# Optimization experiments

Measured on AMD Instinct MI355X. Metric: run time of the kernel, lower is better.

The kernel has to match this reference:

```python
import jax, jax.numpy as jnp
import numpy as np

GROUPS = 8
EPS = 1e-5


def setup_inputs() -> dict:
    key = jax.random.key(0)
    ks = jax.random.split(key, 5)
    b, c, h, w = 16, 512, 64, 64
    x = jax.random.normal(ks[0], (b, c, h, w), dtype=jnp.float32)
    norm_w = jnp.ones((c,), dtype=jnp.float32)
    norm_b = jnp.zeros((c,), dtype=jnp.float32)
    # 1x1 conv weights stored as [out, in] (kernel spatial dims are 1)
    qkv_w = jax.random.normal(ks[1], (3 * c, c), dtype=jnp.float32) * (c ** -0.5)
    qkv_b = jax.random.normal(ks[2], (3 * c,), dtype=jnp.float32) * 0.02
    proj_w = jax.random.normal(ks[3], (c, c), dtype=jnp.float32) * (c ** -0.5)
    proj_b = jax.random.normal(ks[4], (c,), dtype=jnp.float32) * 0.02
    return {"x": x, "norm_w": norm_w, "norm_b": norm_b,
            "qkv_w": qkv_w, "qkv_b": qkv_b, "proj_w": proj_w, "proj_b": proj_b}


def reference(x, norm_w, norm_b, qkv_w, qkv_b, proj_w, proj_b):
    b, c, h, w = x.shape
    n = h * w
    # GroupNorm over (c/groups, h, w) per group, affine per channel
    xg = x.reshape(b, GROUPS, -1)
    mean = xg.mean(axis=-1, keepdims=True)
    var = xg.var(axis=-1, keepdims=True)
    xn = ((xg - mean) * jax.lax.rsqrt(var + EPS)).reshape(b, c, n)
    xn = xn * norm_w[None, :, None] + norm_b[None, :, None]
    # 1x1 conv qkv: [b, 3c, n]
    qkv = jnp.einsum('oc,bcn->bon', qkv_w, xn) + qkv_b[None, :, None]
    qkv = qkv.reshape(b, 3, c, n)
    q, k, v = qkv[:, 0], qkv[:, 1], qkv[:, 2]  # each [b, c, n]
    scale = jnp.asarray(c, x.dtype) ** -0.5
    # NOTE: as in the source, attention is over channels: attn is [b, c, c]
    attn = jnp.einsum('bcn,bdn->bcd', q, k) * scale
    attn = jax.nn.softmax(attn, axis=-1)
    out = jnp.einsum('bcd,bdn->bcn', attn, v)  # [b, c, n]
    out = jnp.einsum('oc,bcn->bon', proj_w, out) + proj_b[None, :, None]
    return x + out.reshape(b, c, h, w)
```

## Files before the change

kernel.cpp:

```cpp
#include <hip/hip_runtime.h>
#include <hip/hip_bf16.h>

using bf16 = __hip_bfloat16;
typedef __attribute__((ext_vector_type(8))) short short8;
typedef __attribute__((ext_vector_type(4))) float f32x4;
typedef __attribute__((ext_vector_type(4))) short short4v;

#define B_   16
#define C_   512
#define N_   4096
#define NG   8
#define GRP_ELEMS (64 * 4096)
static constexpr float kScale = 0.04419417382415922f;
#define SPART_STRIDE 4194304ULL

#define OFF_WQ    0ULL
#define OFF_WP    0x180000ULL
#define OFF_PART  0x204000ULL
#define OFF_SUM   0x210000ULL
#define OFF_CHS   0x218000ULL
#define OFF_U     0x220000ULL
#define OFF_W     0x230000ULL
#define OFF_WVT   0x240000ULL
#define OFF_BV2   0x2C0000ULL
#define OFF_Q     0x400000ULL
#define OFF_K     (OFF_Q  + 0x4000000ULL)
#define OFF_VT    (OFF_K  + 0x4000000ULL)
#define OFF_XNC   OFF_Q
#define OFF_G2    OFF_Q
#define OFF_P     (OFF_Q + 0x1000000ULL)
#define OFF_ATT   (OFF_Q + 0x2000000ULL)
#define OFF_GP    OFF_K
#define OFF_W2    OFF_K
#define OFF_W3    (OFF_K + 0x800000ULL)

typedef __attribute__((address_space(1))) const void* as1cvp;
typedef __attribute__((address_space(3))) void* as3vp;

__device__ inline void gload_lds16(const void* g, void* l) {
  __builtin_amdgcn_global_load_lds((as1cvp)g, (as3vp)l, 16, 0, 0);
}

__device__ inline short bf16bits(float v) {
  bf16 h = __float2bfloat16(v);
  return *reinterpret_cast<short*>(&h);
}

#define BARX() __builtin_amdgcn_s_barrier()
#define SFEN() __builtin_amdgcn_sched_barrier(0)
#define LG0()  asm volatile("s_waitcnt lgkmcnt(0)" ::: "memory")
#define VM4()  asm volatile("s_waitcnt vmcnt(4)" ::: "memory")
#define VM0()  asm volatile("s_waitcnt vmcnt(0)" ::: "memory")

__global__ __launch_bounds__(256) void prep(const float* __restrict__ wq,
                                            const float* __restrict__ wp,
                                            const float* __restrict__ x,
                                            bf16* __restrict__ oq,
                                            bf16* __restrict__ op,
                                            bf16* __restrict__ wvt,
                                            float* __restrict__ part,
                                            float* __restrict__ chansum) {
  if (blockIdx.x < 3072) {
    int i = blockIdx.x * 256 + threadIdx.x;
    oq[i] = __float2bfloat16(wq[i]);
    if (i < 512 * 512) {
      op[i] = __float2bfloat16(wp[i]);
      const int d = i >> 9, c = i & 511;
      wvt[c * 512 + d] = __float2bfloat16(wq[(1024 + d) * 512 + c]);
    }
    return;
  }
  const int bid = blockIdx.x - 3072;
  const int bg  = bid >> 4;
  const int seg = bid & 15;
  const float4* p = (const float4*)(x + (size_t)bg * GRP_ELEMS + seg * 16384);
  float a[4] = {0.f, 0.f, 0.f, 0.f};
  float q = 0.f;
#pragma unroll
  for (int i = 0; i < 16; ++i) {
    float4 v = p[threadIdx.x + i * 256];
    a[i >> 2] += v.x + v.y + v.z + v.w;
    q += v.x * v.x + v.y * v.y + v.z * v.z + v.w * v.w;
  }
  for (int off = 32; off; off >>= 1) {
#pragma unroll
    for (int j = 0; j < 4; ++j) a[j] += __shfl_xor(a[j], off);
    q += __shfl_xor(q, off);
  }
  __shared__ float red[4][5];
  int w = threadIdx.x >> 6;
  if ((threadIdx.x & 63) == 0) {
#pragma unroll
    for (int j = 0; j < 4; ++j) red[w][j] = a[j];
    red[w][4] = q;
  }
  __syncthreads();
  if (threadIdx.x == 0) {
    float c0 = red[0][0] + red[1][0] + red[2][0] + red[3][0];
    float c1 = red[0][1] + red[1][1] + red[2][1] + red[3][1];
    float c2 = red[0][2] + red[1][2] + red[2][2] + red[3][2];
    float c3 = red[0][3] + red[1][3] + red[2][3] + red[3][3];
    float Q  = red[0][4] + red[1][4] + red[2][4] + red[3][4];
    part[bid * 2]     = c0 + c1 + c2 + c3;
    part[bid * 2 + 1] = Q;
    const int b = bg >> 3, c = (bg & 7) * 64 + seg * 4;
    float* cs = chansum + b * 512 + c;
    cs[0] = c0; cs[1] = c1; cs[2] = c2; cs[3] = c3;
  }
}

__global__ __launch_bounds__(256) void gn_apply_t(const float* __restrict__ x,
                                                  const float* __restrict__ part,
                                                  const float* __restrict__ nw,
                                                  const float* __restrict__ nb,
                                                  bf16* __restrict__ xnt,
                                                  bf16* __restrict__ xncn) {
  const int nt = blockIdx.x;
  const int ct = blockIdx.y;
  const int b  = blockIdx.z;
  __shared__ float tile[64][65];
  const int bg = b * NG + ct;
  float Sm = 0.f, Qm = 0.f;
#pragma unroll
  for (int i = 0; i < 16; ++i) {
    Sm += part[(bg * 16 + i) * 2];
    Qm += part[(bg * 16 + i) * 2 + 1];
  }
  const float mean = Sm * (1.f / GRP_ELEMS);
  const float var  = Qm * (1.f / GRP_ELEMS) - mean * mean;
  const float rstd = rsqrtf(var + 1e-5f);

  const int r16 = threadIdx.x >> 4;
  const int q4  = (threadIdx.x & 15) * 4;
#pragma unroll
  for (int p = 0; p < 4; ++p) {
    const int cl = p * 16 + r16;
    const int c  = ct * 64 + cl;
    const float g  = nw[c] * rstd;
    const float sh = nb[c] - mean * g;
    float4 v = *(const float4*)(x + ((size_t)b * C_ + c) * N_ + nt * 64 + q4);
    const float x0 = v.x * g + sh, x1 = v.y * g + sh;
    const float x2 = v.z * g + sh, x3 = v.w * g + sh;
    tile[cl][q4] = x0; tile[cl][q4 + 1] = x1;
    tile[cl][q4 + 2] = x2; tile[cl][q4 + 3] = x3;
    short4v s4 = {bf16bits(x0), bf16bits(x1), bf16bits(x2), bf16bits(x3)};
    *(short4v*)(xncn + ((size_t)b * C_ + c) * N_ + nt * 64 + q4) = s4;
  }
  __syncthreads();
#pragma unroll
  for (int p = 0; p < 4; ++p) {
    const int nl = p * 16 + r16;
    short4v s4 = {bf16bits(tile[q4][nl]), bf16bits(tile[q4 + 1][nl]),
                  bf16bits(tile[q4 + 2][nl]), bf16bits(tile[q4 + 3][nl])};
    *(short4v*)(xnt + ((size_t)b * N_ + nt * 64 + nl) * C_ + ct * 64 + q4) = s4;
  }
}

__global__ __launch_bounds__(512) void mk_ssum(const float* __restrict__ chansum,
                                               const float* __restrict__ part,
                                               const float* __restrict__ nw,
                                               const float* __restrict__ nb,
                                               float* __restrict__ ssum) {
  const int b = blockIdx.x, c = threadIdx.x;
  const int bg = b * NG + (c >> 6);
  float Sm = 0.f, Qm = 0.f;
#pragma unroll
  for (int i = 0; i < 16; ++i) {
    Sm += part[(bg * 16 + i) * 2];
    Qm += part[(bg * 16 + i) * 2 + 1];
  }
  const float mean = Sm * (1.f / GRP_ELEMS);
  const float var  = Qm * (1.f / GRP_ELEMS) - mean * mean;
  const float rstd = rsqrtf(var + 1e-5f);
  const float g  = nw[c] * rstd;
  const float sh = nb[c] - mean * g;
  ssum[b * 512 + c] = g * chansum[b * 512 + c] + 4096.f * sh;
}

__global__ __launch_bounds__(256) void greduce(const float* __restrict__ gp,
                                               bf16* __restrict__ g2) {
  const size_t base = ((size_t)blockIdx.x * 256 + threadIdx.x) * 8;
  float g[8];
#pragma unroll
  for (int j = 0; j < 8; ++j)
    g[j] = gp[base + j] + gp[SPART_STRIDE + base + j] +
           gp[2 * SPART_STRIDE + base + j] + gp[3 * SPART_STRIDE + base + j];
  const int b = (int)(base >> 18), rem = (int)(base & 262143);
  const int e = rem >> 9, k = rem & 511;
  bf16* hi = g2 + ((size_t)b * 512 + e) * 1024 + k;
#pragma unroll
  for (int j = 0; j < 8; ++j) {
    bf16 h = __float2bfloat16(g[j]);
    hi[j]       = h;
    hi[512 + j] = __float2bfloat16(g[j] - __bfloat162float(h));
  }
}

__global__ __launch_bounds__(512) void gemv_uw(const float* __restrict__ qw,
                                               const float* __restrict__ s,
                                               float* __restrict__ u,
                                               float* __restrict__ w) {
  const int b = blockIdx.x >> 1, which = blockIdx.x & 1;
  const int c = threadIdx.x;
  const float* row = qw + (size_t)(which * 512 + c) * 512;
  const float* sv = s + b * 512;
  float acc = 0.f;
  for (int d = 0; d < 512; d += 4) {
    float4 wv = *(const float4*)(row + d);
    float4 s4 = *(const float4*)(sv + d);
    acc += wv.x * s4.x + wv.y * s4.y + wv.z * s4.z + wv.w * s4.w;
  }
  (which ? w : u)[b * 512 + c] = acc;
}

__global__ __launch_bounds__(512) void gemv_bv2(const bf16* __restrict__ w2,
                                                const float* __restrict__ qkv_b,
                                                const float* __restrict__ proj_b,
                                                float* __restrict__ bias2) {
  const int b = blockIdx.x, o = threadIdx.x;
  const bf16* row = w2 + (size_t)b * 262144 + o * 512;
  float acc = proj_b[o];
  for (int d = 0; d < 512; d += 8) {
    short8 v8 = *(const short8*)(row + d);
#pragma unroll
    for (int i = 0; i < 8; ++i) {
      short t = v8[i];
      acc += __bfloat162float(*reinterpret_cast<const bf16*>(&t)) *
             qkv_b[1024 + d + i];
    }
  }
  bias2[b * 512 + o] = acc;
}

template<int MODE>
__global__ __launch_bounds__(512, 2) void gemm8p(
    const bf16* __restrict__ Ag, const bf16* __restrict__ Bg,
    int lda, int ldb, long long sA, long long sB,
    const float* __restrict__ bias,
    void* __restrict__ o0, void* __restrict__ o1, void* __restrict__ o2,
    const float* __restrict__ resid) {
  __shared__ __align__(16) bf16 smem[8][8192];

  constexpr int NIT = (MODE == 1 || MODE == 4) ? 8 : 4;
  const int id = blockIdx.x;
  int bx, by, bz, part;
  if constexpr (MODE == 1) {
    const int s = (id & 7) * 32 + (id >> 3);
    bx = s & 1; by = (s >> 1) & 1; part = (s >> 2) & 3; bz = s >> 4;
  } else if constexpr (MODE == 3) {
    const int s = (id & 7) * 64 + (id >> 3);
    by = s & 1;  bx = (s >> 1) & 15;  bz = s >> 5; part = 0;
  } else {
    const int s = (id & 7) * 8 + (id >> 3);
    bx = s & 1;  by = (s >> 1) & 1;  bz = s >> 2; part = 0;
  }

  const bf16* Apan = Ag + (size_t)bz * sA + (size_t)by * 256 * lda + (size_t)part * 1024;
  const bf16* Bpan = Bg + (size_t)bz * sB + (size_t)bx * 256 * ldb + (size_t)part * 1024;

  const int tid  = threadIdx.x;
  const int lane = tid & 63;
  const int wid  = tid >> 6;
  const int wr   = wid >> 2;
  const int wc   = wid & 3;
  const int mrow = lane & 15, krow = lane >> 4;
  const int wrr  = wr * 64, wcc = wc * 32;

  auto stage = [&](int mat, int buf, int half, int kt) {
    const int ktp = (MODE == 4 && mat == 0) ? (kt & 7) : kt;
    const bf16* gb = mat ? Bpan : Apan;
    const int ld = mat ? ldb : lda;
    char* reg = (char*)smem[mat * 4 + buf * 2 + half];
#pragma unroll
    for (int j = 0; j < 2; ++j) {
      const int idx = j * 512 + tid;
      const int r   = idx >> 3;
      const int c8  = (tid & 7) ^ (r & 7);
      gload_lds16(gb + (size_t)(half * 128 + r) * ld + ktp * 64 + c8 * 8,
                  reg + idx * 16);
    }
  };

  short8 a[4][2], b0[2][2], b1[2][2];
  auto ldA = [&](int buf, int qm) {
    const char* reg = (const char*)smem[buf * 2 + qm];
#pragma unroll
    for (int mi = 0; mi < 4; ++mi) {
      const int lr = wrr + mi * 16 + mrow;
#pragma unroll
      for (int s2 = 0; s2 < 2; ++s2)
        a[mi][s2] = *(const short8*)(reg + lr * 128 +
                                     (((s2 * 4 + krow) ^ (lr & 7)) << 4));
    }
  };
  auto ldB = [&](short8 (&b)[2][2], int buf, int qn) {
    const char* reg = (const char*)smem[4 + buf * 2 + qn];
#pragma unroll
    for (int ni = 0; ni < 2; ++ni) {
      const int lr = wcc + ni * 16 + mrow;
#pragma unroll
      for (int s2 = 0; s2 < 2; ++s2)
        b[ni][s2] = *(const short8*)(reg + lr * 128 +
                                     (((s2 * 4 + krow) ^ (lr & 7)) << 4));
    }
  };

  f32x4 acc[2][2][4][2];
#pragma unroll
  for (int p = 0; p < 2; ++p)
#pragma unroll
    for (int q = 0; q < 2; ++q)
#pragma unroll
      for (int m = 0; m < 4; ++m)
#pragma unroll
        for (int n = 0; n < 2; ++n)
#pragma unroll
          for (int r = 0; r < 4; ++r) acc[p][q][m][n][r] = 0.f;

  auto mm = [&](short8 (&b)[2][2], f32x4 (&c)[4][2]) {
    __builtin_amdgcn_s_setprio(1);
#pragma unroll
    for (int mi = 0; mi < 4; ++mi)
#pragma unroll
      for (int ni = 0; ni < 2; ++ni)
#pragma unroll
        for (int s2 = 0; s2 < 2; ++s2)
          c[mi][ni] = __builtin_amdgcn_mfma_f32_16x16x32_bf16(
              a[mi][s2], b[ni][s2], c[mi][ni], 0, 0, 0);
    __builtin_amdgcn_s_setprio(0);
  };

  stage(0, 0, 0, 0); stage(0, 0, 1, 0); stage(1, 0, 0, 0); stage(1, 0, 1, 0);
  stage(0, 1, 0, 1); stage(1, 1, 0, 1);
  VM4(); BARX(); SFEN();

  for (int i = 0; i < NIT; ++i) {
    const int kt1 = 2 * i + 1, kt2 = 2 * i + 2, kt3 = 2 * i + 3;
    const bool more = (i < NIT - 1);
    ldA(0, 0); ldB(b0, 0, 0); stage(0, 1, 1, kt1);
    BARX(); LG0(); SFEN(); mm(b0, acc[0][0]); BARX();
    ldB(b1, 0, 1); stage(1, 1, 1, kt1);
    BARX(); LG0(); SFEN(); mm(b1, acc[0][1]); BARX();
    ldA(0, 1); if (more) stage(0, 0, 0, kt2);
    BARX(); LG0(); SFEN(); mm(b0, acc[1][0]); BARX();
    if (more) { stage(1, 0, 0, kt2); VM4(); } else { VM0(); }
    BARX(); SFEN(); mm(b1, acc[1][1]); BARX();
    ldA(1, 0); ldB(b0, 1, 0); if (more) stage(0, 0, 1, kt2);
    BARX(); LG0(); SFEN(); mm(b0, acc[0][0]); BARX();
    ldB(b1, 1, 1); if (more) stage(1, 0, 1, kt2);
    BARX(); LG0(); SFEN(); mm(b1, acc[0][1]); BARX();
    ldA(1, 1); if (more) stage(0, 1, 0, kt3);
    BARX(); LG0(); SFEN(); mm(b0, acc[1][0]); BARX();
    if (more) { stage(1, 1, 0, kt3); VM4(); }
    BARX(); SFEN(); mm(b1, acc[1][1]);
    if (more) BARX();
  }

#pragma unroll
  for (int qm = 0; qm < 2; ++qm)
#pragma unroll
  for (int qn = 0; qn < 2; ++qn)
#pragma unroll
  for (int mi = 0; mi < 4; ++mi)
#pragma unroll
  for (int ni = 0; ni < 2; ++ni)
#pragma unroll
  for (int rr = 0; rr < 4; ++rr) {
    const int row_l = qm * 128 + wrr + mi * 16 + krow * 4 + rr;
    const int col_l = qn * 128 + wcc + ni * 16 + mrow;
    float v = acc[qm][qn][mi][ni][rr];
    if constexpr (MODE == 1) {
      const int row = by * 256 + row_l, colg = bx * 256 + col_l;
      ((float*)o0)[(size_t)part * SPART_STRIDE + (size_t)bz * 262144 +
                   row * 512 + colg] = v;
    } else if constexpr (MODE == 2) {
      const int o = by * 256 + row_l, d = bx * 256 + col_l;
      ((bf16*)o0)[(size_t)bz * 262144 + o * 512 + d] = __float2bfloat16(v);
    } else if constexpr (MODE == 3) {
      const int o = by * 256 + row_l;
      const int n = bx * 256 + col_l;
      const size_t addr = ((size_t)bz * C_ + o) * N_ + n;
      ((float*)o0)[addr] = v + bias[(bz << 9) + o] + resid[addr];
    } else if constexpr (MODE == 4) {
      const int c = by * 256 + row_l, e = bx * 256 + col_l;
      ((bf16*)o0)[(size_t)bz * 262144 + c * 512 + e] = __float2bfloat16(v);
    } else {
      const int row = by * 256 + row_l, col = bx * 256 + col_l;
      const float* uu = (const float*)o1;
      const float* ww = (const float*)o2;
      const float bq = bias[row], bk = bias[512 + col];
      const float corr = uu[bz * 512 + row] * bk + bq * ww[bz * 512 + col] +
                         4096.f * bq * bk;
      ((float*)o0)[(size_t)bz * 262144 + row * 512 + col] = (v + corr) * kScale;
    }
  }
}

__global__ __launch_bounds__(256) void softmax_t(const float* __restrict__ S,
                                                 bf16* __restrict__ att_t) {
  const int b  = blockIdx.x >> 4;
  const int ct = blockIdx.x & 15;
  __shared__ bf16 T[512][36];
  const int w = threadIdx.x >> 6, lane = threadIdx.x & 63;
  for (int it = 0; it < 8; ++it) {
    const int cl  = w * 8 + it;
    const int row = b * 512 + ct * 32 + cl;
    const float* p = S + (size_t)row * 512;
    float v[8];
    float mx = -1e30f;
#pragma unroll
    for (int i = 0; i < 8; ++i) { v[i] = p[lane + i * 64]; mx = fmaxf(mx, v[i]); }
    for (int off = 32; off; off >>= 1) mx = fmaxf(mx, __shfl_xor(mx, off));
    float s = 0.f;
#pragma unroll
    for (int i = 0; i < 8; ++i) { v[i] = __expf(v[i] - mx); s += v[i]; }
    for (int off = 32; off; off >>= 1) s += __shfl_xor(s, off);
    float inv = 1.f / s;
#pragma unroll
    for (int i = 0; i < 8; ++i) T[lane + i * 64][cl] = __float2bfloat16(v[i] * inv);
  }
  __syncthreads();
  bf16* outp = att_t + (size_t)b * 262144 + ct * 32;
  const int dof = threadIdx.x >> 3;
  const int c4  = (threadIdx.x & 7) * 4;
  for (int it = 0; it < 16; ++it) {
    const int d = it * 32 + dof;
    *(short4v*)(outp + (size_t)d * 512 + c4) = *(const short4v*)(&T[d][c4]);
  }
}

extern "C" void kernel_launch(void* const* d_in, const int* in_sizes, int n_in,
                              void* d_out, int out_size, void* d_ws, size_t ws_size,
                              hipStream_t stream) {
  const float* x      = (const float*)d_in[0];
  const float* norm_w = (const float*)d_in[1];
  const float* norm_b = (const float*)d_in[2];
  const float* qkv_w  = (const float*)d_in[3];
  const float* qkv_b  = (const float*)d_in[4];
  const float* proj_w = (const float*)d_in[5];
  const float* proj_b = (const float*)d_in[6];
  float* out = (float*)d_out;
  char* ws = (char*)d_ws;

  bf16*  wq    = (bf16*)(ws + OFF_WQ);
  bf16*  wp    = (bf16*)(ws + OFF_WP);
  bf16*  wvt   = (bf16*)(ws + OFF_WVT);
  float* partb = (float*)(ws + OFF_PART);
  float* ssum  = (float*)(ws + OFF_SUM);
  float* chs   = (float*)(ws + OFF_CHS);
  float* u     = (float*)(ws + OFF_U);
  float* wv_   = (float*)(ws + OFF_W);
  float* bias2 = (float*)(ws + OFF_BV2);
  bf16*  xncn  = (bf16*)(ws + OFF_XNC);
  bf16*  g2    = (bf16*)(ws + OFF_G2);
  bf16*  P     = (bf16*)(ws + OFF_P);
  bf16*  att_t = (bf16*)(ws + OFF_ATT);
  float* gpart = (float*)(ws + OFF_GP);
  bf16*  w2    = (bf16*)(ws + OFF_W2);
  bf16*  w3    = (bf16*)(ws + OFF_W3);
  bf16*  xnt   = (bf16*)(ws + OFF_VT);
  float* S     = (float*)d_out;

  prep<<<5120, 256, 0, stream>>>(qkv_w, proj_w, x, wq, wp, wvt, partb, chs);
  gn_apply_t<<<dim3(64, 8, 16), 256, 0, stream>>>(x, partb, norm_w, norm_b,
                                                  xnt, xncn);
  gemm8p<1><<<256, 512, 0, stream>>>(xncn, xncn, 4096, 4096, 2097152LL,
                                     2097152LL, nullptr, gpart, nullptr,
                                     nullptr, nullptr);
  greduce<<<2048, 256, 0, stream>>>(gpart, g2);
  mk_ssum<<<16, 512, 0, stream>>>(chs, partb, norm_w, norm_b, ssum);
  gemv_uw<<<32, 512, 0, stream>>>(qkv_w, ssum, u, wv_);
  gemm8p<4><<<64, 512, 0, stream>>>(wq, g2, 512, 1024, 0, 524288LL,
                                    nullptr, P, nullptr, nullptr, nullptr);
  gemm8p<5><<<64, 512, 0, stream>>>(P, wq + 512 * 512, 512, 512, 262144LL, 0,
                                    qkv_b, S, u, wv_, nullptr);
  softmax_t<<<256, 256, 0, stream>>>(S, att_t);
  gemm8p<2><<<64, 512, 0, stream>>>(wp, att_t, 512, 512, 0, 262144LL,
                                    nullptr, w2, nullptr, nullptr, nullptr);
  gemm8p<2><<<64, 512, 0, stream>>>(w2, wvt, 512, 512, 262144LL, 0,
                                    nullptr, w3, nullptr, nullptr, nullptr);
  gemv_bv2<<<16, 512, 0, stream>>>(w2, qkv_b, proj_b, bias2);
  gemm8p<3><<<512, 512, 0, stream>>>(w3, xnt, 512, 512, 262144LL, 2097152LL,
                                     bias2, out, nullptr, nullptr, x);
}
```

Baseline: 367.5 us.

## Exploit Gram matrix symmetry: compute three of four tiles, mirror the fourth

The per-batch Gram matrix X·Xᵀ (512x512, split into four 256x256 tiles) is symmetric. The gemm launch now computes only the two diagonal tiles and one off-diagonal tile, cutting the split-K GEMM blocks from 256 to 192. The reduction kernel is restructured into 64x64 tiles staged through shared memory, so it can rebuild the missing off-diagonal tile by transposing its mirror. This trades a quarter of the GEMM work for an LDS transpose and a different access pattern in the reduction kernel.

Result: no change. 369.0 us (+0.4%).

```diff
diff --git a/kernel.cpp b/kernel.cpp
--- a/kernel.cpp
+++ b/kernel.cpp
@@ -179,20 +179,36 @@
 
 __global__ __launch_bounds__(256) void greduce(const float* __restrict__ gp,
                                                bf16* __restrict__ g2) {
-  const size_t base = ((size_t)blockIdx.x * 256 + threadIdx.x) * 8;
-  float g[8];
-#pragma unroll
-  for (int j = 0; j < 8; ++j)
-    g[j] = gp[base + j] + gp[SPART_STRIDE + base + j] +
-           gp[2 * SPART_STRIDE + base + j] + gp[3 * SPART_STRIDE + base + j];
-  const int b = (int)(base >> 18), rem = (int)(base & 262143);
-  const int e = rem >> 9, k = rem & 511;
-  bf16* hi = g2 + ((size_t)b * 512 + e) * 1024 + k;
-#pragma unroll
-  for (int j = 0; j < 8; ++j) {
-    bf16 h = __float2bfloat16(g[j]);
+  const int b  = blockIdx.x >> 6;
+  const int t  = blockIdx.x & 63;
+  const int te = t >> 3, tk = t & 7;
+  const bool mir = (te >= 4 && tk < 4);
+  const size_t gbase = (size_t)b * 262144;
+  const int r  = threadIdx.x >> 2;
+  const int c0 = (threadIdx.x & 3) * 16;
+  __shared__ float T[64][65];
+  const int sre = mir ? tk : te, srk = mir ? te : tk;
+  const float* src = gp + gbase + (size_t)(sre * 64 + r) * 512 + srk * 64 + c0;
+#pragma unroll
+  for (int j = 0; j < 16; j += 4) {
+    float4 v0 = *(const float4*)(src + j);
+    float4 v1 = *(const float4*)(src + SPART_STRIDE + j);
+    float4 v2 = *(const float4*)(src + 2 * SPART_STRIDE + j);
+    float4 v3 = *(const float4*)(src + 3 * SPART_STRIDE + j);
+    T[r][c0 + j]     = v0.x + v1.x + v2.x + v3.x;
+    T[r][c0 + j + 1] = v0.y + v1.y + v2.y + v3.y;
+    T[r][c0 + j + 2] = v0.z + v1.z + v2.z + v3.z;
+    T[r][c0 + j + 3] = v0.w + v1.w + v2.w + v3.w;
+  }
+  __syncthreads();
+  const int e = te * 64 + r;
+  bf16* hi = g2 + ((size_t)b * 512 + e) * 1024 + tk * 64 + c0;
+#pragma unroll
+  for (int j = 0; j < 16; ++j) {
+    const float g = mir ? T[c0 + j][r] : T[r][c0 + j];
+    bf16 h = __float2bfloat16(g);
     hi[j]       = h;
-    hi[512 + j] = __float2bfloat16(g[j] - __bfloat162float(h));
+    hi[512 + j] = __float2bfloat16(g - __bfloat162float(h));
   }
 }
 
@@ -245,8 +261,11 @@
   const int id = blockIdx.x;
   int bx, by, bz, part;
   if constexpr (MODE == 1) {
-    const int s = (id & 7) * 32 + (id >> 3);
-    bx = s & 1; by = (s >> 1) & 1; part = (s >> 2) & 3; bz = s >> 4;
+    const int s = (id & 7) * 24 + (id >> 3);
+    const int tile = s % 3, rest = s / 3;
+    part = rest & 3; bz = rest >> 2;
+    by = (tile == 1) ? 1 : 0;
+    bx = (tile == 0) ? 0 : 1;
   } else if constexpr (MODE == 3) {
     const int s = (id & 7) * 64 + (id >> 3);
     by = s & 1;  bx = (s >> 1) & 15;  bz = s >> 5; part = 0;
@@ -464,10 +483,10 @@
   prep<<<5120, 256, 0, stream>>>(qkv_w, proj_w, x, wq, wp, wvt, partb, chs);
   gn_apply_t<<<dim3(64, 8, 16), 256, 0, stream>>>(x, partb, norm_w, norm_b,
                                                   xnt, xncn);
-  gemm8p<1><<<256, 512, 0, stream>>>(xncn, xncn, 4096, 4096, 2097152LL,
+  gemm8p<1><<<192, 512, 0, stream>>>(xncn, xncn, 4096, 4096, 2097152LL,
                                      2097152LL, nullptr, gpart, nullptr,
                                      nullptr, nullptr);
-  greduce<<<2048, 256, 0, stream>>>(gpart, g2);
+  greduce<<<1024, 256, 0, stream>>>(gpart, g2);
   mk_ssum<<<16, 512, 0, stream>>>(chs, partb, norm_w, norm_b, ssum);
   gemv_uw<<<32, 512, 0, stream>>>(qkv_w, ssum, u, wv_);
   gemm8p<4><<<64, 512, 0, stream>>>(wq, g2, 512, 1024, 0, 524288LL,
```
